# Kernel optimization log

Hardware: AMD Instinct MI355X
Metric: run time of the kernel (lower is better)

Reference implementation:

```python
import jax, jax.numpy as jnp
import numpy as np

RS, RC = 3.0, 6.0
N_AXIS = 8
N_NODES, N_ENV, N_EDGES = 50000, 1000000, 200000
N_ATOM = 4
NEURONS = [32, 64, 64]


def setup_inputs() -> dict:
    key = jax.random.key(0)
    ks = jax.random.split(key, 10)
    env_vectors = jax.random.normal(ks[0], (N_ENV, 3), dtype=jnp.float32) * 2.0
    atom_attr = jax.random.uniform(ks[1], (N_NODES, N_ATOM), dtype=jnp.float32)
    env_index = jax.random.randint(ks[2], (2, N_ENV), 0, N_NODES)
    edge_index = jax.random.randint(ks[3], (2, N_EDGES), 0, N_NODES)
    d_in = 2 * N_ATOM + 1  # snorm + both endpoint one-hot attrs
    W1 = jax.random.normal(ks[4], (d_in, NEURONS[0]), dtype=jnp.float32) / np.sqrt(d_in)
    b1 = jnp.zeros((NEURONS[0],), jnp.float32)
    W2 = jax.random.normal(ks[5], (NEURONS[0], NEURONS[1]), dtype=jnp.float32) / np.sqrt(NEURONS[0])
    b2 = jnp.zeros((NEURONS[1],), jnp.float32)
    W3 = jax.random.normal(ks[6], (NEURONS[1], NEURONS[2]), dtype=jnp.float32) / np.sqrt(NEURONS[1])
    b3 = jnp.zeros((NEURONS[2],), jnp.float32)
    return dict(env_vectors=env_vectors, atom_attr=atom_attr, env_index=env_index,
                edge_index=edge_index, W1=W1, b1=b1, W2=W2, b2=b2, W3=W3, b3=b3)


def _smooth(r):
    # elementwise smooth cutoff: 1/r for r<rs, polynomial taper on [rs,rc), 0 beyond
    x = (r - RC) / (RS - RC)
    mid = (1.0 / r) * (x ** 3 * (10.0 + x * (-15.0 + 6.0 * x)) + 1.0)
    return jnp.where(r < RS, 1.0 / r, jnp.where(r < RC, mid, jnp.zeros_like(r)))


def reference(env_vectors, atom_attr, env_index, edge_index, W1, b1, W2, b2, W3, b3):
    n_env = env_vectors.shape[0]
    n_nodes = atom_attr.shape[0]
    r = jnp.linalg.norm(env_vectors, axis=-1, keepdims=True)          # [E,1]
    snorm = _smooth(r)
    # gather both endpoint attrs: env_index.T.flatten() interleaves (src_i, dst_i)
    env_attr = atom_attr[env_index.T.reshape(-1)].reshape(n_env, -1)  # [E, 2*n_atom]
    # ResNet embedding (residual where dims match)
    h = jnp.tanh(jnp.concatenate([snorm, env_attr], axis=-1) @ W1 + b1)
    h = jnp.tanh(h @ W2 + b2)
    h = jnp.tanh(h @ W3 + b3) + h                                     # [E, D]
    # outer product with direction vectors, scatter-mean over target node
    outer = h[:, :, None] * env_vectors[:, None, :]                   # [E, D, 3]
    idx = env_index[1]
    summ = jax.ops.segment_sum(outer, idx, num_segments=n_nodes)      # [N, D, 3]
    cnt = jax.ops.segment_sum(jnp.ones((n_env,), h.dtype), idx, num_segments=n_nodes)
    aggr = summ / jnp.clip(cnt, 1.0)[:, None, None]
    # per-node self outer-product bmm, slice first n_axis columns, flatten
    desc = jnp.einsum('nda,nea->nde', aggr, aggr)[:, :, :N_AXIS]      # [N, D, n_axis]
    node_desc = desc.reshape(n_nodes, -1)                             # [N, D*n_axis]
    edge_desc = node_desc[edge_index[0]] + node_desc[edge_index[1]]   # [Ne, D*n_axis]
    return node_desc, edge_desc
```

## Files before the change

### kernel.cpp

```cpp
#include <hip/hip_runtime.h>
#include <hip/hip_bf16.h>

#define N_NODES 50000
#define N_ENV   1000000
#define N_EDGES 200000

__device__ __forceinline__ float fast_tanh(float x){
  float xc = fminf(fmaxf(x, -10.f), 10.f);
  float t  = __expf(2.f * xc);
  return __fdividef(t - 1.f, t + 1.f);
}

__global__ void k_zero_i(int* __restrict__ p, int n){
  int i = blockIdx.x * blockDim.x + threadIdx.x;
  int stride = gridDim.x * blockDim.x;
  for (; i < n; i += stride) p[i] = 0;
}

__global__ __launch_bounds__(256) void k_hist(
    const int* __restrict__ env_index, int* __restrict__ counts)
{
  int e = blockIdx.x * 256 + threadIdx.x;
  if (e >= N_ENV) return;
  atomicAdd(counts + env_index[N_ENV + e], 1);
}

__global__ __launch_bounds__(64) void k_scan(
    const int* __restrict__ counts, int* __restrict__ offsets,
    int* __restrict__ cursor)
{
  int lane = threadIdx.x;
  int carry = 0;
  for (int base = 0; base < N_NODES; base += 512){
    int i0 = base + lane * 8;
    int c[8];
    #pragma unroll
    for (int j = 0; j < 8; j++){ int i = i0 + j; c[j] = (i < N_NODES) ? counts[i] : 0; }
    int local = 0;
    #pragma unroll
    for (int j = 0; j < 8; j++) local += c[j];
    int incl = local;
    #pragma unroll
    for (int off = 1; off < 64; off <<= 1){
      int t = __shfl_up(incl, off);
      if (lane >= off) incl += t;
    }
    int run = carry + incl - local;
    #pragma unroll
    for (int j = 0; j < 8; j++){
      int i = i0 + j;
      if (i < N_NODES){ offsets[i] = run; cursor[i] = run; }
      run += c[j];
    }
    carry += __shfl(incl, 63);
  }
}

__global__ __launch_bounds__(256) void k_scatter(
    const int* __restrict__ env_index, int* __restrict__ cursor,
    int* __restrict__ order)
{
  int e = blockIdx.x * 256 + threadIdx.x;
  if (e >= N_ENV) return;
  int dst = env_index[N_ENV + e];
  int pos = atomicAdd(cursor + dst, 1);
  order[pos] = e;
}

__global__ __launch_bounds__(256) void k_mlp(
    const float* __restrict__ env_vec, const float* __restrict__ atom_attr,
    const int*  __restrict__ env_index,
    const float* __restrict__ W1, const float* __restrict__ B1,
    const float* __restrict__ W2, const float* __restrict__ B2,
    const float* __restrict__ W3, const float* __restrict__ B3,
    float* __restrict__ h_out)
{
  __shared__ float sW1[32*9];
  __shared__ float sW2[64*32];
  __shared__ float sW3[64*64];
  __shared__ float sB1[32], sB2[64], sB3[64];
  __shared__ float stage[256*17];
  for (int k = threadIdx.x; k < 32*9;  k += 256){ int j = k/9,  i = k%9;  sW1[k] = W1[i*32+j]; }
  for (int k = threadIdx.x; k < 64*32; k += 256){ int j = k>>5, i = k&31; sW2[k] = W2[i*64+j]; }
  for (int k = threadIdx.x; k < 64*64; k += 256){ int j = k>>6, i = k&63; sW3[k] = W3[i*64+j]; }
  if (threadIdx.x < 32) sB1[threadIdx.x] = B1[threadIdx.x];
  if (threadIdx.x < 64) sB2[threadIdx.x] = B2[threadIdx.x];
  if (threadIdx.x < 64) sB3[threadIdx.x] = B3[threadIdx.x];
  __syncthreads();

  int e  = blockIdx.x * 256 + threadIdx.x;
  int el = min(e, N_ENV - 1);

  float v0 = env_vec[3*el+0];
  float v1 = env_vec[3*el+1];
  float v2 = env_vec[3*el+2];
  float r = sqrtf(v0*v0 + v1*v1 + v2*v2);
  float invr = 1.f / r;
  float xx = (r - 6.f) * (-1.f/3.f);
  float mid = invr * (xx*xx*xx*(10.f + xx*(-15.f + 6.f*xx)) + 1.f);
  float snorm = (r < 3.f) ? invr : ((r < 6.f) ? mid : 0.f);

  int src = env_index[el];
  int dst = env_index[N_ENV + el];

  float x[9];
  x[0] = snorm;
  float4 sa = *reinterpret_cast<const float4*>(atom_attr + src*4);
  float4 da = *reinterpret_cast<const float4*>(atom_attr + dst*4);
  x[1]=sa.x; x[2]=sa.y; x[3]=sa.z; x[4]=sa.w;
  x[5]=da.x; x[6]=da.y; x[7]=da.z; x[8]=da.w;

  float h1[32];
  #pragma unroll
  for (int j = 0; j < 32; j++){
    float acc = sB1[j];
    #pragma unroll
    for (int i = 0; i < 9; i++) acc += x[i] * sW1[j*9 + i];
    h1[j] = fast_tanh(acc);
  }

  float h2[64];
  #pragma unroll
  for (int j = 0; j < 64; j++){
    float acc = sB2[j];
    #pragma unroll
    for (int i = 0; i < 32; i++) acc += h1[i] * sW2[j*32 + i];
    h2[j] = fast_tanh(acc);
  }

  const int tid = threadIdx.x;
  #pragma unroll
  for (int c = 0; c < 4; c++){
    #pragma unroll
    for (int dd = 0; dd < 16; dd++){
      int d = c*16 + dd;
      float acc = sB3[d];
      #pragma unroll
      for (int i = 0; i < 64; i++) acc += h2[i] * sW3[d*64 + i];
      stage[tid*17 + dd] = fast_tanh(acc) + h2[d];
    }
    __syncthreads();
    int rb = tid >> 2;
    int j  = tid & 3;
    #pragma unroll
    for (int p = 0; p < 4; p++){
      int rr = p*64 + rb;
      float w0 = stage[rr*17 + j*4 + 0];
      float w1 = stage[rr*17 + j*4 + 1];
      float w2 = stage[rr*17 + j*4 + 2];
      float w3 = stage[rr*17 + j*4 + 3];
      int erow = blockIdx.x * 256 + rr;
      if (erow < N_ENV)
        *reinterpret_cast<float4*>(h_out + (size_t)erow*64 + c*16 + j*4) =
            make_float4(w0, w1, w2, w3);
    }
    __syncthreads();
  }
}

__global__ __launch_bounds__(256) void k_aggr_node(
    const float* __restrict__ h, const float* __restrict__ env_vec,
    const int* __restrict__ offsets, const int* __restrict__ counts,
    const int* __restrict__ order, float* __restrict__ node_out)
{
  int wid  = (blockIdx.x * 256 + threadIdx.x) >> 6;
  int lane = threadIdx.x & 63;
  if (wid >= N_NODES) return;
  int off = offsets[wid];
  int c   = counts[wid];

  float a0 = 0.f, a1 = 0.f, a2 = 0.f;
  int e = (c > 0) ? order[off] : 0;
  for (int k = 0; k < c; k++){
    int eu = __builtin_amdgcn_readfirstlane(e);
    int en = (k + 1 < c) ? order[off + k + 1] : eu;
    float hv = h[(size_t)eu * 64 + lane];
    float v0 = env_vec[3*eu+0];
    float v1 = env_vec[3*eu+1];
    float v2 = env_vec[3*eu+2];
    a0 += hv * v0;
    a1 += hv * v1;
    a2 += hv * v2;
    e = en;
  }
  float inv = 1.f / fmaxf((float)c, 1.f);
  a0 *= inv; a1 *= inv; a2 *= inv;

  float o[8];
  #pragma unroll
  for (int e2 = 0; e2 < 8; e2++){
    float b0 = __shfl(a0, e2);
    float b1 = __shfl(a1, e2);
    float b2 = __shfl(a2, e2);
    o[e2] = a0*b0 + a1*b1 + a2*b2;
  }
  float* dst = node_out + (size_t)wid * 512 + lane * 8;
  *reinterpret_cast<float4*>(dst)     = make_float4(o[0], o[1], o[2], o[3]);
  *reinterpret_cast<float4*>(dst + 4) = make_float4(o[4], o[5], o[6], o[7]);
}

__global__ __launch_bounds__(256) void k_edge(
    const float* __restrict__ node_out, const int* __restrict__ edge_index,
    float* __restrict__ edge_out)
{
  int t = threadIdx.x;
  int e = blockIdx.x * 2 + (t >> 7);
  int l = t & 127;
  int s  = edge_index[e];
  int dn = edge_index[N_EDGES + e];
  const float4* rs = reinterpret_cast<const float4*>(node_out + (size_t)s  * 512);
  const float4* rd = reinterpret_cast<const float4*>(node_out + (size_t)dn * 512);
  float4 a = rs[l];
  float4 b = rd[l];
  float4 o = make_float4(a.x + b.x, a.y + b.y, a.z + b.z, a.w + b.w);
  reinterpret_cast<float4*>(edge_out + (size_t)e * 512)[l] = o;
}

extern "C" void kernel_launch(void* const* d_in, const int* in_sizes, int n_in,
                              void* d_out, int out_size, void* d_ws, size_t ws_size,
                              hipStream_t stream) {
  const float* env_vec    = (const float*)d_in[0];
  const float* atom_attr  = (const float*)d_in[1];
  const int*   env_index  = (const int*)  d_in[2];
  const int*   edge_index = (const int*)  d_in[3];
  const float* W1 = (const float*)d_in[4];
  const float* B1 = (const float*)d_in[5];
  const float* W2 = (const float*)d_in[6];
  const float* B2 = (const float*)d_in[7];
  const float* W3 = (const float*)d_in[8];
  const float* B3 = (const float*)d_in[9];

  float* out      = (float*)d_out;
  float* node_out = out;
  float* edge_out = out + (size_t)N_NODES * 512;

  float* scratch = edge_out;
  float* h       = scratch;
  int*   counts  = (int*)(scratch + 64000000);
  int*   offsets = (int*)(scratch + 64100000);
  int*   cursor  = (int*)(scratch + 64200000);
  int*   order   = (int*)(scratch + 64300000);

  k_zero_i<<<196, 256, 0, stream>>>(counts, N_NODES);

  k_hist<<<(N_ENV + 255) / 256, 256, 0, stream>>>(env_index, counts);

  k_scan<<<1, 64, 0, stream>>>(counts, offsets, cursor);

  k_scatter<<<(N_ENV + 255) / 256, 256, 0, stream>>>(env_index, cursor, order);

  k_mlp<<<(N_ENV + 255) / 256, 256, 0, stream>>>(
      env_vec, atom_attr, env_index, W1, B1, W2, B2, W3, B3, h);

  k_aggr_node<<<(N_NODES + 3) / 4, 256, 0, stream>>>(
      h, env_vec, offsets, counts, order, node_out);

  k_edge<<<N_EDGES / 2, 256, 0, stream>>>(node_out, edge_index, edge_out);
}
```

Measured before the change: 1.355 ms.

## Widen scan to 1024 threads, process two envs per MLP thread, prefetch h rows

The single-wavefront scan becomes a 1024-thread block scan that combines per-wave sums through shared memory, which cuts the number of serial outer iterations. The MLP kernel now evaluates two environment rows per thread so each shared-memory weight load feeds two FMAs, and the launch uses half as many blocks. The aggregation loop prefetches the next h row before it accumulates the current one, so the gather latency overlaps with the arithmetic. The doubled MLP register arrays (h1, h2 for both rows) raise register pressure and may lower occupancy or cause spills.

```diff
diff --git a/kernel.cpp b/kernel.cpp
--- a/kernel.cpp
+++ b/kernel.cpp
@@ -25,14 +25,17 @@
   atomicAdd(counts + env_index[N_ENV + e], 1);
 }
 
-__global__ __launch_bounds__(64) void k_scan(
+__global__ __launch_bounds__(1024) void k_scan(
     const int* __restrict__ counts, int* __restrict__ offsets,
     int* __restrict__ cursor)
 {
-  int lane = threadIdx.x;
-  int carry = 0;
-  for (int base = 0; base < N_NODES; base += 512){
-    int i0 = base + lane * 8;
+  __shared__ int wsum[16];
+  __shared__ int s_carry, s_tot;
+  int tid = threadIdx.x, lane = tid & 63, w = tid >> 6;
+  if (tid == 0) s_carry = 0;
+  __syncthreads();
+  for (int base = 0; base < N_NODES; base += 8192){
+    int i0 = base + tid * 8;
     int c[8];
     #pragma unroll
     for (int j = 0; j < 8; j++){ int i = i0 + j; c[j] = (i < N_NODES) ? counts[i] : 0; }
@@ -45,14 +48,30 @@
       int t = __shfl_up(incl, off);
       if (lane >= off) incl += t;
     }
-    int run = carry + incl - local;
+    if (lane == 63) wsum[w] = incl;
+    __syncthreads();
+    if (w == 0 && lane < 16){
+      int v = wsum[lane];
+      int winc = v;
+      #pragma unroll
+      for (int off = 1; off < 16; off <<= 1){
+        int t = __shfl_up(winc, off);
+        if (lane >= off) winc += t;
+      }
+      wsum[lane] = winc - v;
+      if (lane == 15) s_tot = winc;
+    }
+    __syncthreads();
+    int run = s_carry + wsum[w] + incl - local;
     #pragma unroll
     for (int j = 0; j < 8; j++){
       int i = i0 + j;
       if (i < N_NODES){ offsets[i] = run; cursor[i] = run; }
       run += c[j];
     }
-    carry += __shfl(incl, 63);
+    __syncthreads();
+    if (tid == 0) s_carry += s_tot;
+    __syncthreads();
   }
 }
 
@@ -79,7 +98,7 @@
   __shared__ float sW2[64*32];
   __shared__ float sW3[64*64];
   __shared__ float sB1[32], sB2[64], sB3[64];
-  __shared__ float stage[256*17];
+  __shared__ float stage[512*17];
   for (int k = threadIdx.x; k < 32*9;  k += 256){ int j = k/9,  i = k%9;  sW1[k] = W1[i*32+j]; }
   for (int k = threadIdx.x; k < 64*32; k += 256){ int j = k>>5, i = k&31; sW2[k] = W2[i*64+j]; }
   for (int k = threadIdx.x; k < 64*64; k += 256){ int j = k>>6, i = k&63; sW3[k] = W3[i*64+j]; }
@@ -88,68 +107,83 @@
   if (threadIdx.x < 64) sB3[threadIdx.x] = B3[threadIdx.x];
   __syncthreads();
 
-  int e  = blockIdx.x * 256 + threadIdx.x;
-  int el = min(e, N_ENV - 1);
-
-  float v0 = env_vec[3*el+0];
-  float v1 = env_vec[3*el+1];
-  float v2 = env_vec[3*el+2];
-  float r = sqrtf(v0*v0 + v1*v1 + v2*v2);
-  float invr = 1.f / r;
-  float xx = (r - 6.f) * (-1.f/3.f);
-  float mid = invr * (xx*xx*xx*(10.f + xx*(-15.f + 6.f*xx)) + 1.f);
-  float snorm = (r < 3.f) ? invr : ((r < 6.f) ? mid : 0.f);
-
-  int src = env_index[el];
-  int dst = env_index[N_ENV + el];
-
-  float x[9];
-  x[0] = snorm;
-  float4 sa = *reinterpret_cast<const float4*>(atom_attr + src*4);
-  float4 da = *reinterpret_cast<const float4*>(atom_attr + dst*4);
-  x[1]=sa.x; x[2]=sa.y; x[3]=sa.z; x[4]=sa.w;
-  x[5]=da.x; x[6]=da.y; x[7]=da.z; x[8]=da.w;
-
-  float h1[32];
+  const int tid  = threadIdx.x;
+  const int base = blockIdx.x * 512;
+  int eA = base + tid;
+  int eB = eA + 256;
+  int elA = min(eA, N_ENV - 1);
+  int elB = min(eB, N_ENV - 1);
+
+  float xA[9], xB[9];
+  {
+    float v0 = env_vec[3*elA+0], v1 = env_vec[3*elA+1], v2 = env_vec[3*elA+2];
+    float r = sqrtf(v0*v0 + v1*v1 + v2*v2);
+    float invr = 1.f / r;
+    float xx = (r - 6.f) * (-1.f/3.f);
+    float mid = invr * (xx*xx*xx*(10.f + xx*(-15.f + 6.f*xx)) + 1.f);
+    xA[0] = (r < 3.f) ? invr : ((r < 6.f) ? mid : 0.f);
+    int src = env_index[elA], dst = env_index[N_ENV + elA];
+    float4 sa = *reinterpret_cast<const float4*>(atom_attr + src*4);
+    float4 da = *reinterpret_cast<const float4*>(atom_attr + dst*4);
+    xA[1]=sa.x; xA[2]=sa.y; xA[3]=sa.z; xA[4]=sa.w;
+    xA[5]=da.x; xA[6]=da.y; xA[7]=da.z; xA[8]=da.w;
+  }
+  {
+    float v0 = env_vec[3*elB+0], v1 = env_vec[3*elB+1], v2 = env_vec[3*elB+2];
+    float r = sqrtf(v0*v0 + v1*v1 + v2*v2);
+    float invr = 1.f / r;
+    float xx = (r - 6.f) * (-1.f/3.f);
+    float mid = invr * (xx*xx*xx*(10.f + xx*(-15.f + 6.f*xx)) + 1.f);
+    xB[0] = (r < 3.f) ? invr : ((r < 6.f) ? mid : 0.f);
+    int src = env_index[elB], dst = env_index[N_ENV + elB];
+    float4 sa = *reinterpret_cast<const float4*>(atom_attr + src*4);
+    float4 da = *reinterpret_cast<const float4*>(atom_attr + dst*4);
+    xB[1]=sa.x; xB[2]=sa.y; xB[3]=sa.z; xB[4]=sa.w;
+    xB[5]=da.x; xB[6]=da.y; xB[7]=da.z; xB[8]=da.w;
+  }
+
+  float h1A[32], h1B[32];
   #pragma unroll
   for (int j = 0; j < 32; j++){
-    float acc = sB1[j];
-    #pragma unroll
-    for (int i = 0; i < 9; i++) acc += x[i] * sW1[j*9 + i];
-    h1[j] = fast_tanh(acc);
-  }
-
-  float h2[64];
+    float accA = sB1[j], accB = sB1[j];
+    #pragma unroll
+    for (int i = 0; i < 9; i++){ float w = sW1[j*9 + i]; accA += xA[i]*w; accB += xB[i]*w; }
+    h1A[j] = fast_tanh(accA);
+    h1B[j] = fast_tanh(accB);
+  }
+
+  float h2A[64], h2B[64];
   #pragma unroll
   for (int j = 0; j < 64; j++){
-    float acc = sB2[j];
-    #pragma unroll
-    for (int i = 0; i < 32; i++) acc += h1[i] * sW2[j*32 + i];
-    h2[j] = fast_tanh(acc);
-  }
-
-  const int tid = threadIdx.x;
+    float accA = sB2[j], accB = sB2[j];
+    #pragma unroll
+    for (int i = 0; i < 32; i++){ float w = sW2[j*32 + i]; accA += h1A[i]*w; accB += h1B[i]*w; }
+    h2A[j] = fast_tanh(accA);
+    h2B[j] = fast_tanh(accB);
+  }
+
   #pragma unroll
   for (int c = 0; c < 4; c++){
     #pragma unroll
     for (int dd = 0; dd < 16; dd++){
       int d = c*16 + dd;
-      float acc = sB3[d];
+      float accA = sB3[d], accB = sB3[d];
       #pragma unroll
-      for (int i = 0; i < 64; i++) acc += h2[i] * sW3[d*64 + i];
-      stage[tid*17 + dd] = fast_tanh(acc) + h2[d];
+      for (int i = 0; i < 64; i++){ float w = sW3[d*64 + i]; accA += h2A[i]*w; accB += h2B[i]*w; }
+      stage[tid*17 + dd]       = fast_tanh(accA) + h2A[d];
+      stage[(tid+256)*17 + dd] = fast_tanh(accB) + h2B[d];
     }
     __syncthreads();
     int rb = tid >> 2;
     int j  = tid & 3;
     #pragma unroll
-    for (int p = 0; p < 4; p++){
+    for (int p = 0; p < 8; p++){
       int rr = p*64 + rb;
       float w0 = stage[rr*17 + j*4 + 0];
       float w1 = stage[rr*17 + j*4 + 1];
       float w2 = stage[rr*17 + j*4 + 2];
       float w3 = stage[rr*17 + j*4 + 3];
-      int erow = blockIdx.x * 256 + rr;
+      int erow = base + rr;
       if (erow < N_ENV)
         *reinterpret_cast<float4*>(h_out + (size_t)erow*64 + c*16 + j*4) =
             make_float4(w0, w1, w2, w3);
@@ -170,18 +204,20 @@
   int c   = counts[wid];
 
   float a0 = 0.f, a1 = 0.f, a2 = 0.f;
-  int e = (c > 0) ? order[off] : 0;
-  for (int k = 0; k < c; k++){
-    int eu = __builtin_amdgcn_readfirstlane(e);
-    int en = (k + 1 < c) ? order[off + k + 1] : eu;
-    float hv = h[(size_t)eu * 64 + lane];
-    float v0 = env_vec[3*eu+0];
-    float v1 = env_vec[3*eu+1];
-    float v2 = env_vec[3*eu+2];
-    a0 += hv * v0;
-    a1 += hv * v1;
-    a2 += hv * v2;
-    e = en;
+  if (c > 0){
+    int e = __builtin_amdgcn_readfirstlane(order[off]);
+    float hv = h[(size_t)e * 64 + lane];
+    for (int k = 0; k < c; k++){
+      int en = (k + 1 < c) ? __builtin_amdgcn_readfirstlane(order[off + k + 1]) : e;
+      float hv_n = h[(size_t)en * 64 + lane];
+      float v0 = env_vec[3*e+0];
+      float v1 = env_vec[3*e+1];
+      float v2 = env_vec[3*e+2];
+      a0 += hv * v0;
+      a1 += hv * v1;
+      a2 += hv * v2;
+      e = en; hv = hv_n;
+    }
   }
   float inv = 1.f / fmaxf((float)c, 1.f);
   a0 *= inv; a1 *= inv; a2 *= inv;
@@ -245,11 +281,11 @@
 
   k_hist<<<(N_ENV + 255) / 256, 256, 0, stream>>>(env_index, counts);
 
-  k_scan<<<1, 64, 0, stream>>>(counts, offsets, cursor);
+  k_scan<<<1, 1024, 0, stream>>>(counts, offsets, cursor);
 
   k_scatter<<<(N_ENV + 255) / 256, 256, 0, stream>>>(env_index, cursor, order);
 
-  k_mlp<<<(N_ENV + 255) / 256, 256, 0, stream>>>(
+  k_mlp<<<(N_ENV + 511) / 512, 256, 0, stream>>>(
       env_vec, atom_attr, env_index, W1, B1, W2, B2, W3, B3, h);
 
   k_aggr_node<<<(N_NODES + 3) / 4, 256, 0, stream>>>(
```

After: 1.265 ms. -6.7%, faster.
